# Kernel optimization log

Hardware: AMD Instinct MI355X
Metric: run time of the kernel (lower is better)

Reference implementation:

```python
import jax, jax.numpy as jnp
import numpy as np

N, E, F, H, C, B = 50000, 1_600_000, 128, 128, 10, 512


def setup_inputs() -> dict:
    key = jax.random.key(0)
    ks = jax.random.split(key, 12)
    inp = {
        "x": jax.random.normal(ks[0], (N, F), dtype=jnp.float32),
        "edge_index": jax.random.randint(ks[1], (2, E), 0, N, dtype=jnp.int32),
        "batch": jnp.sort(jax.random.randint(ks[2], (N,), 0, B, dtype=jnp.int32)),
        "edge_weight": jax.random.uniform(ks[3], (E,), dtype=jnp.float32),
        "W1": jax.random.normal(ks[4], (F, H), dtype=jnp.float32) * 0.05,
        "b1": jnp.zeros((H,), dtype=jnp.float32),
        "W2": jax.random.normal(ks[5], (H, H), dtype=jnp.float32) * 0.05,
        "b2": jnp.zeros((H,), dtype=jnp.float32),
        "W3": jax.random.normal(ks[6], (H, H), dtype=jnp.float32) * 0.05,
        "b3": jnp.zeros((H,), dtype=jnp.float32),
        "Wlin": jax.random.normal(ks[7], (H, C), dtype=jnp.float32) * 0.05,
        "blin": jnp.zeros((C,), dtype=jnp.float32),
    }
    return inp


def reference(x, edge_index, batch, edge_weight, W1, b1, W2, b2, W3, b3, Wlin, blin):
    n = x.shape[0]
    src, dst = edge_index[0], edge_index[1]
    loops = jnp.arange(n, dtype=src.dtype)
    src_f = jnp.concatenate([src, loops])  # edges + self-loops
    dst_f = jnp.concatenate([dst, loops])

    def make_norm(fill_value):
        # GCN symmetric normalization: D^-1/2 (A + fill*I) D^-1/2 on edge weights
        ew = jnp.concatenate([edge_weight, jnp.full((n,), fill_value, dtype=edge_weight.dtype)])
        deg = jax.ops.segment_sum(ew, dst_f, num_segments=n)
        dinv = jnp.where(deg > 0, deg ** -0.5, 0.0)
        return dinv[src_f] * ew * dinv[dst_f]

    # conv1 was built as GCNConv(in, hidden, out_channels) -> third positional arg is
    # `improved`, truthy => self-loop fill value 2.0; conv2/3 use 1.0.
    norm1 = make_norm(2.0)
    norm = make_norm(1.0)

    def gcn_conv(h, W, b, nrm):
        h = h @ W                                   # [N, H]
        msg = h[src_f] * nrm[:, None]               # [E+N, H] gather
        return jax.ops.segment_sum(msg, dst_f, num_segments=n) + b

    h = jax.nn.relu(gcn_conv(x, W1, b1, norm1))
    h = jax.nn.relu(gcn_conv(h, W2, b2, norm))
    h = gcn_conv(h, W3, b3, norm)

    # global_mean_pool over graph ids
    sums = jax.ops.segment_sum(h, batch, num_segments=B)
    cnt = jax.ops.segment_sum(jnp.ones((n,), dtype=h.dtype), batch, num_segments=B)
    pooled = sums / jnp.maximum(cnt, 1.0)[:, None]

    # dropout is identity in eval mode
    return pooled @ Wlin + blin
```

## Files before the change

### kernel.cpp

```cpp
#include <hip/hip_runtime.h>
#include <hip/hip_fp16.h>

#define F 128
#define HID 128
#define NCLS 10
#define CAP 80
#define NBIN 256
#define NPB 196
#define SCAP 7168
#define EPT 8
#define HLS 136

typedef short short8 __attribute__((ext_vector_type(8)));
typedef float float4v __attribute__((ext_vector_type(4)));

__device__ __forceinline__ unsigned short f2bf(float f) {
    unsigned int u = __float_as_uint(f);
    unsigned int r = (u + 0x7FFFu + ((u >> 16) & 1u)) >> 16;
    return (unsigned short)r;
}
__device__ __forceinline__ float bf2f(unsigned int h) {
    return __uint_as_float(h << 16);
}

__global__ void prep_misc_kernel(const float* __restrict__ W1,
                                 const float* __restrict__ W2,
                                 const float* __restrict__ W3,
                                 const float* __restrict__ Wlin,
                                 const float* __restrict__ blin,
                                 const float* __restrict__ b3,
                                 unsigned short* __restrict__ Wp,
                                 unsigned short* __restrict__ Wp3s,
                                 float* __restrict__ bL,
                                 int* __restrict__ gcur) {
    int b = blockIdx.x;
    int tid = threadIdx.x;
    if (b < 128) {
        int widx = b >> 6;
        const float* W = (widx == 0) ? W1 : W2;
        int idx = (b & 63) * 256 + tid;
        int j = idx & 7;
        int l = (idx >> 3) & 63;
        int nt = (idx >> 9) & 7;
        int kt = idx >> 12;
        int k = kt * 32 + ((l >> 4) << 3) + j;
        int n = nt * 16 + (l & 15);
        Wp[widx * 16384 + idx] = f2bf(W[k * HID + n]);
    } else if (b < 136) {
        int idx = (b - 128) * 256 + tid;
        int j = idx & 7;
        int l = (idx >> 3) & 63;
        int kt = idx >> 9;
        int k = kt * 32 + ((l >> 4) << 3) + j;
        int n = l & 15;
        float v = 0.f;
        if (n < NCLS) {
            for (int m = 0; m < HID; m++)
                v += W3[k * HID + m] * Wlin[m * NCLS + n];
        }
        Wp3s[idx] = f2bf(v);
    } else {
        gcur[tid] = 0;
        if (tid < NCLS) {
            float bl = blin[tid];
            for (int j = 0; j < HID; j++) bl += b3[j] * Wlin[j * NCLS + tid];
            bL[tid] = bl;
        }
    }
}

__global__ __launch_bounds__(256) void bin_edges(const int* __restrict__ ei,
                                                 const float* __restrict__ ew,
                                                 int* __restrict__ gcur,
                                                 uint2* __restrict__ staging, int E) {
    __shared__ int lhist[NBIN];
    __shared__ int lbase[NBIN];
    int tid = threadIdx.x;
    lhist[tid] = 0;
    __syncthreads();

    unsigned int rpk[EPT];
    unsigned short rd[EPT];
    unsigned short rloc[EPT];
    int base = blockIdx.x * (256 * EPT);
#pragma unroll
    for (int i = 0; i < EPT; i++) {
        int e = base + tid + i * 256;
        if (e < E) {
            int s = ei[e];
            int d = ei[E + e];
            unsigned int q = (unsigned int)(ew[e] * 65535.0f + 0.5f);
            rpk[i] = (q << 16) | (unsigned int)s;
            rd[i] = (unsigned short)d;
            rloc[i] = (unsigned short)atomicAdd(&lhist[d / NPB], 1);
        } else {
            rpk[i] = 0u; rd[i] = 0; rloc[i] = 0;
        }
    }
    __syncthreads();
    lbase[tid] = atomicAdd(&gcur[tid], lhist[tid]);
    __syncthreads();

#pragma unroll
    for (int i = 0; i < EPT; i++) {
        int e = base + tid + i * 256;
        if (e < E) {
            int bin = (int)rd[i] / NPB;
            int pos = lbase[bin] + (int)rloc[i];
            if (pos < SCAP)
                staging[(size_t)bin * SCAP + pos] =
                    make_uint2(rpk[i], (unsigned int)rd[i]);
        }
    }
}

__global__ __launch_bounds__(1024) void build_buckets(const uint2* __restrict__ staging,
                                                      const int* __restrict__ gcur,
                                                      unsigned int* __restrict__ colw,
                                                      int* __restrict__ cnt,
                                                      float* __restrict__ dinv1,
                                                      float* __restrict__ dinv0, int N) {
    __shared__ unsigned int lbuck[NPB * CAP];
    __shared__ int lcnt[NPB];
    int tid = threadIdx.x;
    int bin = blockIdx.x;
    int node0 = bin * NPB;

    for (int n = tid; n < NPB; n += 1024) lcnt[n] = 0;
    __syncthreads();

    int bcnt = gcur[bin];
    if (bcnt > SCAP) bcnt = SCAP;
    const uint2* st = staging + (size_t)bin * SCAP;
    for (int i = tid; i < bcnt; i += 1024) {
        uint2 t = st[i];
        int dl = (int)t.y - node0;
        int pos = atomicAdd(&lcnt[dl], 1);
        if (pos < CAP) lbuck[dl * CAP + pos] = t.x;
    }
    __syncthreads();

    for (int it = 0; it < NPB; it += 128) {
        int nl = it + (tid >> 3);
        int lane = tid & 7;
        if (nl < NPB) {
            int gn = node0 + nl;
            if (gn < N) {
                int c = lcnt[nl];
                if (c > CAP) c = CAP;
                float s = 0.f;
                for (int j = lane; j < c; j += 8)
                    s += (float)(lbuck[nl * CAP + j] >> 16);
                s += __shfl_down(s, 4, 8);
                s += __shfl_down(s, 2, 8);
                s += __shfl_down(s, 1, 8);
                if (lane == 0) {
                    float deg = s * (1.0f / 65535.0f);
                    cnt[gn] = c;
                    dinv1[gn] = 1.0f / sqrtf(deg + 2.0f);
                    dinv0[gn] = 1.0f / sqrtf(deg + 1.0f);
                }
            }
        }
    }
    __syncthreads();

    int nvalid = N - node0;
    if (nvalid > NPB) nvalid = NPB;
    if (nvalid <= 0) return;
    int nslots = nvalid * (CAP / 4);
    uint4* dst4 = (uint4*)(colw + (size_t)node0 * CAP);
    const uint4* src4 = (const uint4*)lbuck;
    for (int i = tid; i < nslots; i += 1024) {
        int rowi = i / (CAP / 4);
        int slot = i - rowi * (CAP / 4);
        int c = lcnt[rowi];
        if (c > CAP) c = CAP;
        if (slot * 4 < c) dst4[i] = src4[i];
    }
}

__global__ __launch_bounds__(256) void gemm_mfma_f32_kernel(const float* __restrict__ X,
                                                            const unsigned short* __restrict__ Wp,
                                                            unsigned short* __restrict__ Yb,
                                                            int N) {
    __shared__ unsigned short Wl[16384];
    __shared__ unsigned short Ol[4][16 * 128];

    int tid = threadIdx.x;
    const uint4* Wp4 = (const uint4*)Wp;
    uint4* Wl4 = (uint4*)Wl;
#pragma unroll
    for (int i = 0; i < 8; i++)
        Wl4[tid + i * 256] = Wp4[tid + i * 256];
    __syncthreads();

    int wave = tid >> 6, lane = tid & 63;
    int quad = lane >> 4, m = lane & 15;
    int row0 = blockIdx.x * 64 + wave * 16;
    int row = row0 + m;
    int rowc = row < N ? row : N - 1;

    short8 a[4];
    const float4* xrow = (const float4*)(X + (size_t)rowc * F);
#pragma unroll
    for (int kt = 0; kt < 4; kt++) {
        float4 p0 = xrow[kt * 8 + quad * 2];
        float4 p1 = xrow[kt * 8 + quad * 2 + 1];
        short8 v;
        v[0] = (short)f2bf(p0.x); v[1] = (short)f2bf(p0.y);
        v[2] = (short)f2bf(p0.z); v[3] = (short)f2bf(p0.w);
        v[4] = (short)f2bf(p1.x); v[5] = (short)f2bf(p1.y);
        v[6] = (short)f2bf(p1.z); v[7] = (short)f2bf(p1.w);
        a[kt] = v;
    }

    float4v acc[8];
#pragma unroll
    for (int nt = 0; nt < 8; nt++) {
        float4v c = {0.f, 0.f, 0.f, 0.f};
#pragma unroll
        for (int kt = 0; kt < 4; kt++) {
            short8 b = *(const short8*)(Wl + (((kt * 8 + nt) * 64 + lane) << 3));
            c = __builtin_amdgcn_mfma_f32_16x16x32_bf16(a[kt], b, c, 0, 0, 0);
        }
        acc[nt] = c;
    }

    unsigned short* ol = &Ol[wave][0];
#pragma unroll
    for (int nt = 0; nt < 8; nt++)
#pragma unroll
        for (int r = 0; r < 4; r++)
            ol[(quad * 4 + r) * HID + nt * 16 + m] = f2bf(acc[nt][r]);
    __syncthreads();

#pragma unroll
    for (int it = 0; it < 4; it++) {
        int off = it * 1024 + lane * 16;
        int r = off >> 8;
        int gr = row0 + r;
        if (gr < N) {
            uint4 v = *(const uint4*)((const char*)ol + off);
            *(uint4*)((char*)Yb + (size_t)gr * 256 + (off & 255)) = v;
        }
    }
}

__device__ __forceinline__ void agg_slot(unsigned int pk, int cc, int lane,
                                         const uint2* __restrict__ hin2,
                                         float& ax, float& ay, float& az, float& aw) {
    int jj = 0;
    for (; jj + 8 <= cc; jj += 8) {
        unsigned int w[8];
        uint2 h[8];
#pragma unroll
        for (int t = 0; t < 8; t++)
            w[t] = (unsigned int)__shfl((int)pk, jj + t, 32);
#pragma unroll
        for (int t = 0; t < 8; t++)
            h[t] = hin2[(w[t] & 0xFFFFu) * 32 + lane];
#pragma unroll
        for (int t = 0; t < 8; t++) {
            float f = __half2float(__ushort_as_half((unsigned short)(w[t] >> 16)));
            ax += f * bf2f(h[t].x & 0xFFFFu);
            ay += f * bf2f(h[t].x >> 16);
            az += f * bf2f(h[t].y & 0xFFFFu);
            aw += f * bf2f(h[t].y >> 16);
        }
    }
    if (jj + 4 <= cc) {
        unsigned int w[4];
        uint2 h[4];
#pragma unroll
        for (int t = 0; t < 4; t++)
            w[t] = (unsigned int)__shfl((int)pk, jj + t, 32);
#pragma unroll
        for (int t = 0; t < 4; t++)
            h[t] = hin2[(w[t] & 0xFFFFu) * 32 + lane];
#pragma unroll
        for (int t = 0; t < 4; t++) {
            float f = __half2float(__ushort_as_half((unsigned short)(w[t] >> 16)));
            ax += f * bf2f(h[t].x & 0xFFFFu);
            ay += f * bf2f(h[t].x >> 16);
            az += f * bf2f(h[t].y & 0xFFFFu);
            aw += f * bf2f(h[t].y >> 16);
        }
        jj += 4;
    }
    for (; jj < cc; jj++) {
        unsigned int w = (unsigned int)__shfl((int)pk, jj, 32);
        uint2 hv = hin2[(w & 0xFFFFu) * 32 + lane];
        float f = __half2float(__ushort_as_half((unsigned short)(w >> 16)));
        ax += f * bf2f(hv.x & 0xFFFFu);
        ay += f * bf2f(hv.x >> 16);
        az += f * bf2f(hv.y & 0xFFFFu);
        aw += f * bf2f(hv.y >> 16);
    }
}

__device__ __forceinline__ uint2 agg_node(int g, int lane,
                                          const unsigned short* __restrict__ hin,
                                          const unsigned int* __restrict__ colw,
                                          const int* __restrict__ cnt,
                                          const float* __restrict__ dinv,
                                          float fill, const float* __restrict__ bias) {
    float dv = dinv[g];
    int c = cnt[g];
    if (c > CAP) c = CAP;
    const unsigned int* row = colw + (size_t)g * CAP;
    const uint2* hin2 = (const uint2*)hin;

    unsigned int pk[3];
#pragma unroll
    for (int k = 0; k < 3; k++) {
        int idx = lane + k * 32;
        unsigned int e = (idx < c) ? row[idx] : 0u;
        int s = (int)(e & 0xFFFFu);
        float wf = (float)(e >> 16) * (1.0f / 65535.0f) * dinv[s];
        unsigned short hw = __half_as_ushort(__float2half(wf));
        pk[k] = (e & 0xFFFFu) | ((unsigned int)hw << 16);
    }

    float ax = 0.f, ay = 0.f, az = 0.f, aw = 0.f;
    int c0 = c < 32 ? c : 32;
    agg_slot(pk[0], c0, lane, hin2, ax, ay, az, aw);
    if (c > 32) {
        int c1 = (c - 32) < 32 ? (c - 32) : 32;
        agg_slot(pk[1], c1, lane, hin2, ax, ay, az, aw);
        if (c > 64) agg_slot(pk[2], c - 64, lane, hin2, ax, ay, az, aw);
    }

    uint2 hv = hin2[(size_t)g * 32 + lane];
    float wself = fill * dv;
    ax = (ax + wself * bf2f(hv.x & 0xFFFFu)) * dv;
    ay = (ay + wself * bf2f(hv.x >> 16)) * dv;
    az = (az + wself * bf2f(hv.y & 0xFFFFu)) * dv;
    aw = (aw + wself * bf2f(hv.y >> 16)) * dv;

    float4 b = ((const float4*)bias)[lane];
    ax += b.x; ay += b.y; az += b.z; aw += b.w;
    ax = fmaxf(ax, 0.f); ay = fmaxf(ay, 0.f);
    az = fmaxf(az, 0.f); aw = fmaxf(aw, 0.f);
    uint2 o;
    o.x = (unsigned int)f2bf(ax) | ((unsigned int)f2bf(ay) << 16);
    o.y = (unsigned int)f2bf(az) | ((unsigned int)f2bf(aw) << 16);
    return o;
}

__global__ __launch_bounds__(512) void agg_gemm128_kernel(const unsigned short* __restrict__ hin,
                                                          const unsigned int* __restrict__ colw,
                                                          const int* __restrict__ cnt,
                                                          const float* __restrict__ dinv,
                                                          const float* __restrict__ bias,
                                                          const unsigned short* __restrict__ Wp2,
                                                          unsigned short* __restrict__ Yb,
                                                          int N) {
    __shared__ unsigned short hl[16 * HLS];
    __shared__ unsigned short Ol[16 * 128];

    int tid = threadIdx.x;
    int gl = tid >> 5, lane = tid & 31;
    int row0 = blockIdx.x * 16;
    int g = row0 + gl;

    uint2 o = make_uint2(0u, 0u);
    if (g < N) o = agg_node(g, lane, hin, colw, cnt, dinv, 2.0f, bias);
    *(uint2*)(hl + gl * HLS + lane * 4) = o;
    __syncthreads();

    int nt = tid >> 6;
    int lane64 = tid & 63;
    int quad = lane64 >> 4, m = lane64 & 15;

    short8 a[4];
#pragma unroll
    for (int kt = 0; kt < 4; kt++)
        a[kt] = *(const short8*)(hl + m * HLS + kt * 32 + quad * 8);

    float4v c = {0.f, 0.f, 0.f, 0.f};
#pragma unroll
    for (int kt = 0; kt < 4; kt++) {
        short8 b = *(const short8*)(Wp2 + (((kt * 8 + nt) * 64 + lane64) << 3));
        c = __builtin_amdgcn_mfma_f32_16x16x32_bf16(a[kt], b, c, 0, 0, 0);
    }
#pragma unroll
    for (int r = 0; r < 4; r++)
        Ol[(quad * 4 + r) * HID + nt * 16 + m] = f2bf(c[r]);
    __syncthreads();

    if (tid < 256) {
        int gr = row0 + (tid >> 4);
        if (gr < N)
            ((uint4*)((char*)Yb + (size_t)gr * 256))[tid & 15] = ((const uint4*)Ol)[tid];
    }
}

__global__ __launch_bounds__(512) void agg_gemm16_kernel(const unsigned short* __restrict__ hin,
                                                         const unsigned int* __restrict__ colw,
                                                         const int* __restrict__ cnt,
                                                         const float* __restrict__ dinv,
                                                         const float* __restrict__ bias,
                                                         const unsigned short* __restrict__ Wp3s,
                                                         unsigned short* __restrict__ g3s,
                                                         int N) {
    __shared__ unsigned short hl[16 * HLS];

    int tid = threadIdx.x;
    int gl = tid >> 5, lane = tid & 31;
    int row0 = blockIdx.x * 16;
    int g = row0 + gl;

    uint2 o = make_uint2(0u, 0u);
    if (g < N) o = agg_node(g, lane, hin, colw, cnt, dinv, 1.0f, bias);
    *(uint2*)(hl + gl * HLS + lane * 4) = o;
    __syncthreads();

    if (tid < 64) {
        int lane64 = tid;
        int quad = lane64 >> 4, m = lane64 & 15;
        short8 a[4];
#pragma unroll
        for (int kt = 0; kt < 4; kt++)
            a[kt] = *(const short8*)(hl + m * HLS + kt * 32 + quad * 8);
        float4v c = {0.f, 0.f, 0.f, 0.f};
#pragma unroll
        for (int kt = 0; kt < 4; kt++) {
            short8 b = *(const short8*)(Wp3s + ((kt * 64 + lane64) << 3));
            c = __builtin_amdgcn_mfma_f32_16x16x32_bf16(a[kt], b, c, 0, 0, 0);
        }
#pragma unroll
        for (int r = 0; r < 4; r++) {
            int gr = row0 + quad * 4 + r;
            if (gr < N) g3s[(size_t)gr * 16 + m] = f2bf(c[r]);
        }
    }
}

__device__ __forceinline__ void agg3_slot(unsigned int pk, int cc, int lane2off,
                                          const unsigned short* __restrict__ g3s,
                                          float& ax, float& ay) {
    if (cc == 8) {
        unsigned int w[8];
        unsigned int h[8];
#pragma unroll
        for (int t = 0; t < 8; t++)
            w[t] = (unsigned int)__shfl((int)pk, t, 8);
#pragma unroll
        for (int t = 0; t < 8; t++)
            h[t] = *(const unsigned int*)(g3s + (w[t] & 0xFFFFu) * 16 + lane2off);
#pragma unroll
        for (int t = 0; t < 8; t++) {
            float f = __half2float(__ushort_as_half((unsigned short)(w[t] >> 16)));
            ax += f * bf2f(h[t] & 0xFFFFu);
            ay += f * bf2f(h[t] >> 16);
        }
    } else {
        for (int t = 0; t < cc; t++) {
            unsigned int w = (unsigned int)__shfl((int)pk, t, 8);
            unsigned int h = *(const unsigned int*)(g3s + (w & 0xFFFFu) * 16 + lane2off);
            float f = __half2float(__ushort_as_half((unsigned short)(w >> 16)));
            ax += f * bf2f(h & 0xFFFFu);
            ay += f * bf2f(h >> 16);
        }
    }
}

__global__ __launch_bounds__(256) void agg3_kernel(const unsigned short* __restrict__ g3s,
                                                   const unsigned int* __restrict__ colw,
                                                   const int* __restrict__ cnt,
                                                   const float* __restrict__ dinv,
                                                   unsigned short* __restrict__ h3s, int N) {
    int g = (blockIdx.x * blockDim.x + threadIdx.x) >> 3;
    int lane = threadIdx.x & 7;
    if (g >= N) return;

    float dv = dinv[g];
    int c = cnt[g];
    if (c > CAP) c = CAP;
    const unsigned int* row = colw + (size_t)g * CAP;
    int lane2off = lane * 2;

    unsigned int pk[10];
#pragma unroll
    for (int k = 0; k < 10; k++) {
        int idx = lane + k * 8;
        unsigned int e = (idx < c) ? row[idx] : 0u;
        int s = (int)(e & 0xFFFFu);
        float wf = (float)(e >> 16) * (1.0f / 65535.0f) * dinv[s];
        unsigned short hw = __half_as_ushort(__float2half(wf));
        pk[k] = (e & 0xFFFFu) | ((unsigned int)hw << 16);
    }

    float ax = 0.f, ay = 0.f;
#pragma unroll
    for (int slot = 0; slot < 10; slot++) {
        int base = slot * 8;
        if (c > base) {
            int cc = c - base;
            if (cc > 8) cc = 8;
            agg3_slot(pk[slot], cc, lane2off, g3s, ax, ay);
        }
    }

    unsigned int hv = *(const unsigned int*)(g3s + (size_t)g * 16 + lane2off);
    ax = (ax + dv * bf2f(hv & 0xFFFFu)) * dv;
    ay = (ay + dv * bf2f(hv >> 16)) * dv;

    unsigned int o = (unsigned int)f2bf(ax) | ((unsigned int)f2bf(ay) << 16);
    *(unsigned int*)(h3s + (size_t)g * 16 + lane2off) = o;
}

__global__ __launch_bounds__(256) void pool3_kernel(const unsigned short* __restrict__ h3s,
                                                    const int* __restrict__ batch,
                                                    const float* __restrict__ bL,
                                                    const float* __restrict__ blin,
                                                    float* __restrict__ out, int N, int B) {
    int wave = (blockIdx.x * blockDim.x + threadIdx.x) >> 6;
    int lane = threadIdx.x & 63;
    if (wave >= B) return;
    int g = wave;
    int d = lane & 15, sub = lane >> 4;

    int lo = 0, hi = N;
    while (lo < hi) { int m = (lo + hi) >> 1; if (batch[m] < g) lo = m + 1; else hi = m; }
    int s0 = lo;
    hi = N;
    while (lo < hi) { int m = (lo + hi) >> 1; if (batch[m] < g + 1) lo = m + 1; else hi = m; }
    int s1 = lo;

    float p = 0.f;
    for (int v = s0 + sub; v < s1; v += 4)
        p += bf2f((unsigned int)h3s[(size_t)v * 16 + d]);
    p += __shfl_down(p, 32, 64);
    p += __shfl_down(p, 16, 64);

    if (lane < NCLS) {
        int cntv = s1 - s0;
        float r = (cntv > 0) ? (p / (float)cntv + bL[d]) : blin[d];
        out[g * NCLS + d] = r;
    }
}

extern "C" void kernel_launch(void* const* d_in, const int* in_sizes, int n_in,
                              void* d_out, int out_size, void* d_ws, size_t ws_size,
                              hipStream_t stream) {
    const float* x    = (const float*)d_in[0];
    const int*   ei   = (const int*)d_in[1];
    const int*   batch= (const int*)d_in[2];
    const float* ew   = (const float*)d_in[3];
    const float* W1   = (const float*)d_in[4];
    const float* b1   = (const float*)d_in[5];
    const float* W2   = (const float*)d_in[6];
    const float* b2   = (const float*)d_in[7];
    const float* W3   = (const float*)d_in[8];
    const float* b3   = (const float*)d_in[9];
    const float* Wlin = (const float*)d_in[10];
    const float* blin = (const float*)d_in[11];
    float* out = (float*)d_out;

    int N = in_sizes[0] / F;
    int E = in_sizes[1] / 2;
    int B = out_size / NCLS;

    char* p = (char*)d_ws;
    auto alloc = [&](size_t bytes) -> void* {
        void* r = (void*)p;
        p += (bytes + 255) & ~(size_t)255;
        return r;
    };
    int*            cnt   = (int*)alloc((size_t)N * 4);
    float*          dinv1 = (float*)alloc((size_t)N * 4);
    float*          dinv0 = (float*)alloc((size_t)N * 4);
    int*            gcur  = (int*)alloc(NBIN * 4);
    float*          bL    = (float*)alloc(16 * 4);
    unsigned int*   colw  = (unsigned int*)alloc((size_t)N * CAP * 4);
    unsigned short* Wp    = (unsigned short*)alloc(2 * 16384 * 2);
    unsigned short* Wp3s  = (unsigned short*)alloc(2048 * 2);
    unsigned short* bufA  = (unsigned short*)alloc((size_t)N * HID * 2);
    unsigned short* bufB  = (unsigned short*)alloc((size_t)N * HID * 2);
    unsigned short* g3s   = (unsigned short*)alloc((size_t)N * 16 * 2);
    unsigned short* h3s   = (unsigned short*)alloc((size_t)N * 16 * 2);
    uint2* staging = (uint2*)bufA;

    int tb = 256;
    int nbins = (N + NPB - 1) / NPB;
    prep_misc_kernel<<<137, tb, 0, stream>>>(W1, W2, W3, Wlin, blin, b3, Wp, Wp3s, bL, gcur);
    bin_edges<<<(E + tb * EPT - 1) / (tb * EPT), tb, 0, stream>>>(ei, ew, gcur, staging, E);
    build_buckets<<<nbins, 1024, 0, stream>>>(staging, gcur, colw, cnt, dinv1, dinv0, N);

    int gemm_blocks = (N + 63) / 64;
    int fused_blocks = (N + 15) / 16;
    int agg3_blocks = ((N * 8) + tb - 1) / tb;

    gemm_mfma_f32_kernel<<<gemm_blocks, tb, 0, stream>>>(x, Wp, bufA, N);
    agg_gemm128_kernel<<<fused_blocks, 512, 0, stream>>>(bufA, colw, cnt, dinv1, b1,
                                                         Wp + 16384, bufB, N);
    agg_gemm16_kernel<<<fused_blocks, 512, 0, stream>>>(bufB, colw, cnt, dinv0, b2,
                                                        Wp3s, g3s, N);
    agg3_kernel<<<agg3_blocks, tb, 0, stream>>>(g3s, colw, cnt, dinv0, h3s, N);
    pool3_kernel<<<((B * 64) + tb - 1) / tb, tb, 0, stream>>>(h3s, batch, bL, blin,
                                                              out, N, B);
}
```

Before: 288.9 us.

## Fuse weight prep into edge binning and layer-1 GEMM into bucket build

Weight packing and bias folding now run as extra blocks of the edge-binning kernel. The layer-1 bf16 MFMA GEMM now runs as extra blocks of the bucket-build kernel, and the gcur counters are cleared with a memset instead. Staging gets its own buffer so the GEMM can write bufA while buckets are built. The aim is fewer kernel launches and overlap of the independent stages. In exchange, the GEMM reads B fragments straight from global memory instead of LDS. It writes its output as scattered 2-byte stores instead of coalesced 16-byte rows, and it shares the large LDS footprint and 1024-thread block shape of the build kernel.

```diff
diff --git a/kernel.cpp b/kernel.cpp
--- a/kernel.cpp
+++ b/kernel.cpp
@@ -23,226 +23,193 @@
     return __uint_as_float(h << 16);
 }
 
-__global__ void prep_misc_kernel(const float* __restrict__ W1,
-                                 const float* __restrict__ W2,
-                                 const float* __restrict__ W3,
-                                 const float* __restrict__ Wlin,
-                                 const float* __restrict__ blin,
-                                 const float* __restrict__ b3,
-                                 unsigned short* __restrict__ Wp,
-                                 unsigned short* __restrict__ Wp3s,
-                                 float* __restrict__ bL,
-                                 int* __restrict__ gcur) {
-    int b = blockIdx.x;
-    int tid = threadIdx.x;
-    if (b < 128) {
-        int widx = b >> 6;
-        const float* W = (widx == 0) ? W1 : W2;
-        int idx = (b & 63) * 256 + tid;
-        int j = idx & 7;
-        int l = (idx >> 3) & 63;
-        int nt = (idx >> 9) & 7;
-        int kt = idx >> 12;
-        int k = kt * 32 + ((l >> 4) << 3) + j;
-        int n = nt * 16 + (l & 15);
-        Wp[widx * 16384 + idx] = f2bf(W[k * HID + n]);
-    } else if (b < 136) {
-        int idx = (b - 128) * 256 + tid;
-        int j = idx & 7;
-        int l = (idx >> 3) & 63;
-        int kt = idx >> 9;
-        int k = kt * 32 + ((l >> 4) << 3) + j;
-        int n = l & 15;
-        float v = 0.f;
-        if (n < NCLS) {
-            for (int m = 0; m < HID; m++)
-                v += W3[k * HID + m] * Wlin[m * NCLS + n];
-        }
-        Wp3s[idx] = f2bf(v);
-    } else {
-        gcur[tid] = 0;
-        if (tid < NCLS) {
-            float bl = blin[tid];
-            for (int j = 0; j < HID; j++) bl += b3[j] * Wlin[j * NCLS + tid];
-            bL[tid] = bl;
-        }
-    }
-}
-
-__global__ __launch_bounds__(256) void bin_edges(const int* __restrict__ ei,
-                                                 const float* __restrict__ ew,
-                                                 int* __restrict__ gcur,
-                                                 uint2* __restrict__ staging, int E) {
+__global__ __launch_bounds__(256) void bin_prep_kernel(
+    const int* __restrict__ ei, const float* __restrict__ ew,
+    int* __restrict__ gcur, uint2* __restrict__ staging, int E, int nbb,
+    const float* __restrict__ W1, const float* __restrict__ W2,
+    const float* __restrict__ W3, const float* __restrict__ Wlin,
+    const float* __restrict__ blin, const float* __restrict__ b3,
+    unsigned short* __restrict__ Wp, unsigned short* __restrict__ Wp3s,
+    float* __restrict__ bL) {
     __shared__ int lhist[NBIN];
     __shared__ int lbase[NBIN];
     int tid = threadIdx.x;
-    lhist[tid] = 0;
-    __syncthreads();
-
-    unsigned int rpk[EPT];
-    unsigned short rd[EPT];
-    unsigned short rloc[EPT];
-    int base = blockIdx.x * (256 * EPT);
-#pragma unroll
-    for (int i = 0; i < EPT; i++) {
-        int e = base + tid + i * 256;
-        if (e < E) {
-            int s = ei[e];
-            int d = ei[E + e];
-            unsigned int q = (unsigned int)(ew[e] * 65535.0f + 0.5f);
-            rpk[i] = (q << 16) | (unsigned int)s;
-            rd[i] = (unsigned short)d;
-            rloc[i] = (unsigned short)atomicAdd(&lhist[d / NPB], 1);
+
+    if ((int)blockIdx.x < nbb) {
+        lhist[tid] = 0;
+        __syncthreads();
+
+        unsigned int rpk[EPT];
+        unsigned short rd[EPT];
+        unsigned short rloc[EPT];
+        int base = blockIdx.x * (256 * EPT);
+#pragma unroll
+        for (int i = 0; i < EPT; i++) {
+            int e = base + tid + i * 256;
+            if (e < E) {
+                int s = ei[e];
+                int d = ei[E + e];
+                unsigned int q = (unsigned int)(ew[e] * 65535.0f + 0.5f);
+                rpk[i] = (q << 16) | (unsigned int)s;
+                rd[i] = (unsigned short)d;
+                rloc[i] = (unsigned short)atomicAdd(&lhist[d / NPB], 1);
+            } else {
+                rpk[i] = 0u; rd[i] = 0; rloc[i] = 0;
+            }
+        }
+        __syncthreads();
+        lbase[tid] = atomicAdd(&gcur[tid], lhist[tid]);
+        __syncthreads();
+
+#pragma unroll
+        for (int i = 0; i < EPT; i++) {
+            int e = base + tid + i * 256;
+            if (e < E) {
+                int bin = (int)rd[i] / NPB;
+                int pos = lbase[bin] + (int)rloc[i];
+                if (pos < SCAP)
+                    staging[(size_t)bin * SCAP + pos] =
+                        make_uint2(rpk[i], (unsigned int)rd[i]);
+            }
+        }
+    } else {
+        int b = blockIdx.x - nbb;
+        if (b < 128) {
+            int widx = b >> 6;
+            const float* W = (widx == 0) ? W1 : W2;
+            int idx = (b & 63) * 256 + tid;
+            int j = idx & 7;
+            int l = (idx >> 3) & 63;
+            int nt = (idx >> 9) & 7;
+            int kt = idx >> 12;
+            int k = kt * 32 + ((l >> 4) << 3) + j;
+            int n = nt * 16 + (l & 15);
+            Wp[widx * 16384 + idx] = f2bf(W[k * HID + n]);
+        } else if (b < 136) {
+            int idx = (b - 128) * 256 + tid;
+            int j = idx & 7;
+            int l = (idx >> 3) & 63;
+            int kt = idx >> 9;
+            int k = kt * 32 + ((l >> 4) << 3) + j;
+            int n = l & 15;
+            float v = 0.f;
+            if (n < NCLS) {
+                for (int m = 0; m < HID; m++)
+                    v += W3[k * HID + m] * Wlin[m * NCLS + n];
+            }
+            Wp3s[idx] = f2bf(v);
         } else {
-            rpk[i] = 0u; rd[i] = 0; rloc[i] = 0;
-        }
-    }
-    __syncthreads();
-    lbase[tid] = atomicAdd(&gcur[tid], lhist[tid]);
-    __syncthreads();
-
-#pragma unroll
-    for (int i = 0; i < EPT; i++) {
-        int e = base + tid + i * 256;
-        if (e < E) {
-            int bin = (int)rd[i] / NPB;
-            int pos = lbase[bin] + (int)rloc[i];
-            if (pos < SCAP)
-                staging[(size_t)bin * SCAP + pos] =
-                    make_uint2(rpk[i], (unsigned int)rd[i]);
-        }
-    }
-}
-
-__global__ __launch_bounds__(1024) void build_buckets(const uint2* __restrict__ staging,
-                                                      const int* __restrict__ gcur,
-                                                      unsigned int* __restrict__ colw,
-                                                      int* __restrict__ cnt,
-                                                      float* __restrict__ dinv1,
-                                                      float* __restrict__ dinv0, int N) {
+            if (tid < NCLS) {
+                float bl = blin[tid];
+                for (int j = 0; j < HID; j++) bl += b3[j] * Wlin[j * NCLS + tid];
+                bL[tid] = bl;
+            }
+        }
+    }
+}
+
+__global__ __launch_bounds__(1024, 8) void build_gemm1_kernel(
+    const uint2* __restrict__ staging, const int* __restrict__ gcur,
+    unsigned int* __restrict__ colw, int* __restrict__ cnt,
+    float* __restrict__ dinv1, float* __restrict__ dinv0, int N, int nbins,
+    const float* __restrict__ X, const unsigned short* __restrict__ Wp,
+    unsigned short* __restrict__ Yb) {
     __shared__ unsigned int lbuck[NPB * CAP];
     __shared__ int lcnt[NPB];
     int tid = threadIdx.x;
-    int bin = blockIdx.x;
-    int node0 = bin * NPB;
-
-    for (int n = tid; n < NPB; n += 1024) lcnt[n] = 0;
-    __syncthreads();
-
-    int bcnt = gcur[bin];
-    if (bcnt > SCAP) bcnt = SCAP;
-    const uint2* st = staging + (size_t)bin * SCAP;
-    for (int i = tid; i < bcnt; i += 1024) {
-        uint2 t = st[i];
-        int dl = (int)t.y - node0;
-        int pos = atomicAdd(&lcnt[dl], 1);
-        if (pos < CAP) lbuck[dl * CAP + pos] = t.x;
-    }
-    __syncthreads();
-
-    for (int it = 0; it < NPB; it += 128) {
-        int nl = it + (tid >> 3);
-        int lane = tid & 7;
-        if (nl < NPB) {
-            int gn = node0 + nl;
-            if (gn < N) {
-                int c = lcnt[nl];
-                if (c > CAP) c = CAP;
-                float s = 0.f;
-                for (int j = lane; j < c; j += 8)
-                    s += (float)(lbuck[nl * CAP + j] >> 16);
-                s += __shfl_down(s, 4, 8);
-                s += __shfl_down(s, 2, 8);
-                s += __shfl_down(s, 1, 8);
-                if (lane == 0) {
-                    float deg = s * (1.0f / 65535.0f);
-                    cnt[gn] = c;
-                    dinv1[gn] = 1.0f / sqrtf(deg + 2.0f);
-                    dinv0[gn] = 1.0f / sqrtf(deg + 1.0f);
+
+    if ((int)blockIdx.x < nbins) {
+        int bin = blockIdx.x;
+        int node0 = bin * NPB;
+
+        for (int n = tid; n < NPB; n += 1024) lcnt[n] = 0;
+        __syncthreads();
+
+        int bcnt = gcur[bin];
+        if (bcnt > SCAP) bcnt = SCAP;
+        const uint2* st = staging + (size_t)bin * SCAP;
+        for (int i = tid; i < bcnt; i += 1024) {
+            uint2 t = st[i];
+            int dl = (int)t.y - node0;
+            int pos = atomicAdd(&lcnt[dl], 1);
+            if (pos < CAP) lbuck[dl * CAP + pos] = t.x;
+        }
+        __syncthreads();
+
+        for (int it = 0; it < NPB; it += 128) {
+            int nl = it + (tid >> 3);
+            int lane = tid & 7;
+            if (nl < NPB) {
+                int gn = node0 + nl;
+                if (gn < N) {
+                    int c = lcnt[nl];
+                    if (c > CAP) c = CAP;
+                    float s = 0.f;
+                    for (int j = lane; j < c; j += 8)
+                        s += (float)(lbuck[nl * CAP + j] >> 16);
+                    s += __shfl_down(s, 4, 8);
+                    s += __shfl_down(s, 2, 8);
+                    s += __shfl_down(s, 1, 8);
+                    if (lane == 0) {
+                        float deg = s * (1.0f / 65535.0f);
+                        cnt[gn] = c;
+                        dinv1[gn] = 1.0f / sqrtf(deg + 2.0f);
+                        dinv0[gn] = 1.0f / sqrtf(deg + 1.0f);
+                    }
                 }
             }
         }
-    }
-    __syncthreads();
-
-    int nvalid = N - node0;
-    if (nvalid > NPB) nvalid = NPB;
-    if (nvalid <= 0) return;
-    int nslots = nvalid * (CAP / 4);
-    uint4* dst4 = (uint4*)(colw + (size_t)node0 * CAP);
-    const uint4* src4 = (const uint4*)lbuck;
-    for (int i = tid; i < nslots; i += 1024) {
-        int rowi = i / (CAP / 4);
-        int slot = i - rowi * (CAP / 4);
-        int c = lcnt[rowi];
-        if (c > CAP) c = CAP;
-        if (slot * 4 < c) dst4[i] = src4[i];
-    }
-}
-
-__global__ __launch_bounds__(256) void gemm_mfma_f32_kernel(const float* __restrict__ X,
-                                                            const unsigned short* __restrict__ Wp,
-                                                            unsigned short* __restrict__ Yb,
-                                                            int N) {
-    __shared__ unsigned short Wl[16384];
-    __shared__ unsigned short Ol[4][16 * 128];
-
-    int tid = threadIdx.x;
-    const uint4* Wp4 = (const uint4*)Wp;
-    uint4* Wl4 = (uint4*)Wl;
-#pragma unroll
-    for (int i = 0; i < 8; i++)
-        Wl4[tid + i * 256] = Wp4[tid + i * 256];
-    __syncthreads();
-
-    int wave = tid >> 6, lane = tid & 63;
-    int quad = lane >> 4, m = lane & 15;
-    int row0 = blockIdx.x * 64 + wave * 16;
-    int row = row0 + m;
-    int rowc = row < N ? row : N - 1;
-
-    short8 a[4];
-    const float4* xrow = (const float4*)(X + (size_t)rowc * F);
-#pragma unroll
-    for (int kt = 0; kt < 4; kt++) {
-        float4 p0 = xrow[kt * 8 + quad * 2];
-        float4 p1 = xrow[kt * 8 + quad * 2 + 1];
-        short8 v;
-        v[0] = (short)f2bf(p0.x); v[1] = (short)f2bf(p0.y);
-        v[2] = (short)f2bf(p0.z); v[3] = (short)f2bf(p0.w);
-        v[4] = (short)f2bf(p1.x); v[5] = (short)f2bf(p1.y);
-        v[6] = (short)f2bf(p1.z); v[7] = (short)f2bf(p1.w);
-        a[kt] = v;
-    }
-
-    float4v acc[8];
-#pragma unroll
-    for (int nt = 0; nt < 8; nt++) {
-        float4v c = {0.f, 0.f, 0.f, 0.f};
+        __syncthreads();
+
+        int nvalid = N - node0;
+        if (nvalid > NPB) nvalid = NPB;
+        if (nvalid <= 0) return;
+        int nslots = nvalid * (CAP / 4);
+        uint4* dst4 = (uint4*)(colw + (size_t)node0 * CAP);
+        const uint4* src4 = (const uint4*)lbuck;
+        for (int i = tid; i < nslots; i += 1024) {
+            int rowi = i / (CAP / 4);
+            int slot = i - rowi * (CAP / 4);
+            int c = lcnt[rowi];
+            if (c > CAP) c = CAP;
+            if (slot * 4 < c) dst4[i] = src4[i];
+        }
+    } else {
+        int tile = blockIdx.x - nbins;
+        int wave = tid >> 6, lane = tid & 63;
+        int quad = lane >> 4, m = lane & 15;
+        int row0 = tile * 256 + wave * 16;
+        if (row0 >= N) return;
+        int row = row0 + m;
+        int rowc = row < N ? row : N - 1;
+
+        short8 a[4];
+        const float4* xrow = (const float4*)(X + (size_t)rowc * F);
 #pragma unroll
         for (int kt = 0; kt < 4; kt++) {
-            short8 b = *(const short8*)(Wl + (((kt * 8 + nt) * 64 + lane) << 3));
-            c = __builtin_amdgcn_mfma_f32_16x16x32_bf16(a[kt], b, c, 0, 0, 0);
-        }
-        acc[nt] = c;
-    }
-
-    unsigned short* ol = &Ol[wave][0];
-#pragma unroll
-    for (int nt = 0; nt < 8; nt++)
-#pragma unroll
-        for (int r = 0; r < 4; r++)
-            ol[(quad * 4 + r) * HID + nt * 16 + m] = f2bf(acc[nt][r]);
-    __syncthreads();
-
-#pragma unroll
-    for (int it = 0; it < 4; it++) {
-        int off = it * 1024 + lane * 16;
-        int r = off >> 8;
-        int gr = row0 + r;
-        if (gr < N) {
-            uint4 v = *(const uint4*)((const char*)ol + off);
-            *(uint4*)((char*)Yb + (size_t)gr * 256 + (off & 255)) = v;
+            float4 p0 = xrow[kt * 8 + quad * 2];
+            float4 p1 = xrow[kt * 8 + quad * 2 + 1];
+            short8 v;
+            v[0] = (short)f2bf(p0.x); v[1] = (short)f2bf(p0.y);
+            v[2] = (short)f2bf(p0.z); v[3] = (short)f2bf(p0.w);
+            v[4] = (short)f2bf(p1.x); v[5] = (short)f2bf(p1.y);
+            v[6] = (short)f2bf(p1.z); v[7] = (short)f2bf(p1.w);
+            a[kt] = v;
+        }
+
+#pragma unroll
+        for (int nt = 0; nt < 8; nt++) {
+            float4v c = {0.f, 0.f, 0.f, 0.f};
+#pragma unroll
+            for (int kt = 0; kt < 4; kt++) {
+                short8 b = *(const short8*)(Wp + (((kt * 8 + nt) * 64 + lane) << 3));
+                c = __builtin_amdgcn_mfma_f32_16x16x32_bf16(a[kt], b, c, 0, 0, 0);
+            }
+#pragma unroll
+            for (int r = 0; r < 4; r++) {
+                int gr = row0 + quad * 4 + r;
+                if (gr < N) Yb[(size_t)gr * HID + nt * 16 + m] = f2bf(c[r]);
+            }
         }
     }
 }
@@ -581,19 +548,24 @@
     unsigned short* bufB  = (unsigned short*)alloc((size_t)N * HID * 2);
     unsigned short* g3s   = (unsigned short*)alloc((size_t)N * 16 * 2);
     unsigned short* h3s   = (unsigned short*)alloc((size_t)N * 16 * 2);
-    uint2* staging = (uint2*)bufA;
+    uint2*          staging = (uint2*)alloc((size_t)NBIN * SCAP * 8);
 
     int tb = 256;
     int nbins = (N + NPB - 1) / NPB;
-    prep_misc_kernel<<<137, tb, 0, stream>>>(W1, W2, W3, Wlin, blin, b3, Wp, Wp3s, bL, gcur);
-    bin_edges<<<(E + tb * EPT - 1) / (tb * EPT), tb, 0, stream>>>(ei, ew, gcur, staging, E);
-    build_buckets<<<nbins, 1024, 0, stream>>>(staging, gcur, colw, cnt, dinv1, dinv0, N);
-
-    int gemm_blocks = (N + 63) / 64;
+    int nbb = (E + tb * EPT - 1) / (tb * EPT);
+    int g1tiles = (N + 255) / 256;
+
+    hipMemsetAsync(gcur, 0, NBIN * 4, stream);
+    bin_prep_kernel<<<nbb + 137, tb, 0, stream>>>(ei, ew, gcur, staging, E, nbb,
+                                                  W1, W2, W3, Wlin, blin, b3,
+                                                  Wp, Wp3s, bL);
+    build_gemm1_kernel<<<nbins + g1tiles, 1024, 0, stream>>>(staging, gcur, colw, cnt,
+                                                             dinv1, dinv0, N, nbins,
+                                                             x, Wp, bufA);
+
     int fused_blocks = (N + 15) / 16;
     int agg3_blocks = ((N * 8) + tb - 1) / tb;
 
-    gemm_mfma_f32_kernel<<<gemm_blocks, tb, 0, stream>>>(x, Wp, bufA, N);
     agg_gemm128_kernel<<<fused_blocks, 512, 0, stream>>>(bufA, colw, cnt, dinv1, b1,
                                                          Wp + 16384, bufB, N);
     agg_gemm16_kernel<<<fused_blocks, 512, 0, stream>>>(bufB, colw, cnt, dinv0, b2,
```

New measurement: 289.4 us. No clear change (+0.2%).
